# Kernel tuning notes

Hardware: AMD Instinct MI355X
Metric: run time of the kernel (lower is better)

Reference implementation:

```python
import jax, jax.numpy as jnp
import numpy as np

B, F_, J, D = 64, 256, 25, 3
FILT = 64
N = B * F_ * J
EPS = 1e-5


def setup_inputs() -> dict:
    key = jax.random.key(0)
    ks = jax.random.split(key, 20)
    x = jax.random.normal(ks[0], (B, F_, J, D), jnp.float32)
    # block-diagonal skeleton: chain bones, bidirectional, tiled over B*F graphs
    bones = np.stack([np.arange(J - 1), np.arange(1, J)], axis=1)  # (24,2)
    e = np.concatenate([bones, bones[:, ::-1]], axis=0)            # (48,2)
    G = B * F_
    off = (np.arange(G, dtype=np.int64) * J)[:, None, None]
    edge_index = jnp.asarray((e[None].astype(np.int64) + off).reshape(-1, 2).T)  # (2, G*48)
    s = 0.1
    W1 = jax.random.normal(ks[1], (D, FILT), jnp.float32) * s
    b1 = jnp.zeros((FILT,), jnp.float32)
    g1 = jnp.ones((FILT,), jnp.float32)
    be1 = jnp.zeros((FILT,), jnp.float32)
    W2 = jax.random.normal(ks[2], (FILT, FILT), jnp.float32) * s
    b2 = jnp.zeros((FILT,), jnp.float32)
    g2 = jnp.ones((FILT,), jnp.float32)
    be2 = jnp.zeros((FILT,), jnp.float32)
    cw1 = jax.random.normal(ks[3], (2 * FILT, J * FILT, 3), jnp.float32) * 0.02  # OIH
    cb1 = jnp.zeros((2 * FILT,), jnp.float32)
    cg1 = jnp.ones((2 * FILT,), jnp.float32)
    cbe1 = jnp.zeros((2 * FILT,), jnp.float32)
    cw2 = jax.random.normal(ks[4], (FILT, 2 * FILT, 1), jnp.float32) * 0.05
    cb2 = jnp.zeros((FILT,), jnp.float32)
    cg2 = jnp.ones((FILT,), jnp.float32)
    cbe2 = jnp.zeros((FILT,), jnp.float32)
    return dict(x=x, edge_index=edge_index, batch_size=B, frame_l=F_,
                W1=W1, b1=b1, g1=g1, be1=be1, W2=W2, b2=b2, g2=g2, be2=be2,
                cw1=cw1, cb1=cb1, cg1=cg1, cbe1=cbe1,
                cw2=cw2, cb2=cb2, cg2=cg2, cbe2=cbe2)


def _lrelu(v):
    return jnp.where(v >= 0, v, 0.2 * v)


def _bn_nodes(v, g, b):  # BatchNorm1d on (N, C), batch stats
    m = v.mean(0)
    var = v.var(0)
    return g * (v - m) * jax.lax.rsqrt(var + EPS) + b


def _bn_ncl(v, g, b):  # BatchNorm1d on (B, C, L), batch stats
    m = v.mean((0, 2), keepdims=True)
    var = v.var((0, 2), keepdims=True)
    return g[None, :, None] * (v - m) * jax.lax.rsqrt(var + EPS) + b[None, :, None]


def _gcn(h_in, W, b, src, dst, n):
    # PyG GCNConv: h' = D^{-1/2} (A+I) D^{-1/2} h W + b
    h = h_in @ W
    loop = jnp.arange(n, dtype=src.dtype)
    sa = jnp.concatenate([src, loop])
    da = jnp.concatenate([dst, loop])
    deg = jax.ops.segment_sum(jnp.ones(sa.shape[0], h.dtype), da, num_segments=n)
    dinv = jnp.where(deg > 0, jax.lax.rsqrt(deg), 0.0)
    norm = dinv[sa] * dinv[da]
    return jax.ops.segment_sum(h[sa] * norm[:, None], da, num_segments=n) + b


def _conv1d(v, w, pad):  # v:(B,C,L), w:(O,I,K)
    return jax.lax.conv_general_dilated(v, w, window_strides=(1,), padding=((pad, pad),),
                                         dimension_numbers=("NCH", "OIH", "NCH"))


def reference(x, edge_index, batch_size, frame_l, W1, b1, g1, be1, W2, b2, g2, be2,
              cw1, cb1, cg1, cbe1, cw2, cb2, cg2, cbe2):
    src, dst = edge_index[0], edge_index[1]
    n = x.shape[0] * x.shape[1] * x.shape[2]
    h = x.reshape(-1, x.shape[-1])                               # (N, D)
    h = _lrelu(_bn_nodes(_gcn(h, W1, b1, src, dst, n), g1, be1))  # (N, FILT)
    h = _lrelu(_bn_nodes(_gcn(h, W2, b2, src, dst, n), g2, be2))  # (N, FILT)
    t = h.reshape(batch_size, frame_l, -1).transpose(0, 2, 1)     # (B, J*FILT, L)
    t = _lrelu(_bn_ncl(_conv1d(t, cw1, 1) + cb1[None, :, None], cg1, cbe1))  # dropout: eval = identity
    t = _lrelu(_bn_ncl(_conv1d(t, cw2, 0) + cb2[None, :, None], cg2, cbe2))
    return t.transpose(0, 2, 1)                                   # (B, L, FILT)
```

## Files before the change

### kernel.cpp

```cpp
#include <hip/hip_runtime.h>
#include <stdint.h>

#define B_ 64
#define F2_ 256
#define J_ 25
#define FILT_ 64
#define C1_ 1600
#define O1_ 128
#define NN_ 409600
#define MM_ 16384
#define EPSV 1e-5f

typedef short short8 __attribute__((ext_vector_type(8)));
typedef float f32x4 __attribute__((ext_vector_type(4)));

static const size_t WS_Y2T  = 0;
static const size_t WS_XA   = 52838400;
static const size_t WS_WT1  = 57753600;
static const size_t WS_WT2  = 58982400;
static const size_t WS_WT2G = 58998784;
static const size_t WS_Y3   = 59006976;
static const size_t WS_Y4   = 67395584;
static const size_t WS_ST   = 71589888;
#define ST_S9    0
#define ST_SUM2  16
#define ST_SQ2   80
#define ST_SUM3  144
#define ST_SQ3   272
#define ST_SUM4  400
#define ST_SQ4   464
#define ST_S1    528
#define ST_T1    592
#define ST_SC2   656
#define ST_SH2   720
#define ST_SC3   784
#define ST_SH3   912
#define ST_SC4   1040
#define ST_SH4   1104
#define ST_COUNT 1168

__device__ __forceinline__ float bf2f(unsigned int u){
  return __uint_as_float(u << 16);
}
__device__ __forceinline__ unsigned short f2bf(float f){
  unsigned int u = __float_as_uint(f);
  u += 0x7fffu + ((u >> 16) & 1u);
  return (unsigned short)(u >> 16);
}
__device__ __forceinline__ float lrelu(float x){ return fmaxf(x, 0.2f * x); }
__device__ __forceinline__ float wsum(float v){
  #pragma unroll
  for (int off = 32; off > 0; off >>= 1) v += __shfl_down(v, off, 64);
  return v;
}

typedef __attribute__((address_space(3))) unsigned int lds_uint_t;
typedef __attribute__((address_space(1))) const unsigned int glob_uint_t;
__device__ __forceinline__ void gl16(const void* g, void* l){
  __builtin_amdgcn_global_load_lds((glob_uint_t*)g, (lds_uint_t*)l, 16, 0, 0);
}

__global__ __launch_bounds__(256) void k_zpad(unsigned short* __restrict__ y2t){
  int b = blockIdx.x, tid = threadIdx.x;
  if (tid < 200){
    uint4 z = make_uint4(0,0,0,0);
    ((uint4*)(y2t + (size_t)b * 412800))[tid] = z;
    ((uint4*)(y2t + (size_t)b * 412800 + 257 * 1600))[tid] = z;
  }
}

__global__ __launch_bounds__(256) void k_wt(const float* __restrict__ cw1,
                                            const float* __restrict__ W2,
                                            const float* __restrict__ cw2,
                                            unsigned short* __restrict__ wt1,
                                            unsigned short* __restrict__ wt2,
                                            unsigned short* __restrict__ wt2g){
  int blk = blockIdx.x;
  if (blk < 384){
    int k = blk >> 7, o = blk & 127;
    for (int c = threadIdx.x; c < 1600; c += 256)
      wt1[(size_t)(k * 128 + o) * 1600 + c] = f2bf(cw1[(size_t)(o * 1600 + c) * 3 + k]);
  } else if (blk < 416){
    int idx = ((blk - 384) << 8) + threadIdx.x;
    wt2[idx] = f2bf(cw2[idx]);
  } else {
    int idx = ((blk - 416) << 8) + threadIdx.x;
    int f = idx >> 6, cc = idx & 63;
    wt2g[idx] = f2bf(W2[cc * 64 + f]);
  }
}

__global__ __launch_bounds__(256) void k_gcn1(const float* __restrict__ x,
                                              float* __restrict__ xa,
                                              float* __restrict__ S9){
  int n = blockIdx.x * 256 + threadIdx.x;
  int j = n % J_;
  float dj  = (j == 0 || j == J_-1) ? 2.f : 3.f;
  float rdj = rsqrtf(dj);
  const float* xp = x + (size_t)n * 3;
  float wg = 1.f / dj;
  float a0 = xp[0]*wg, a1 = xp[1]*wg, a2 = xp[2]*wg;
  if (j > 0){
    float dm = (j == 1) ? 2.f : 3.f;  float w = rdj * rsqrtf(dm);
    a0 += xp[-3]*w; a1 += xp[-2]*w; a2 += xp[-1]*w;
  }
  if (j < J_-1){
    float dp = (j == J_-2) ? 2.f : 3.f;  float w = rdj * rsqrtf(dp);
    a0 += xp[3]*w; a1 += xp[4]*w; a2 += xp[5]*w;
  }
  float* xo = xa + (size_t)n * 3;
  xo[0] = a0; xo[1] = a1; xo[2] = a2;
  float p[9] = {a0, a1, a2, a0*a0, a0*a1, a0*a2, a1*a1, a1*a2, a2*a2};
  __shared__ float tmp[9][4];
  int wv = threadIdx.x >> 6, ln = threadIdx.x & 63;
  #pragma unroll
  for (int k = 0; k < 9; k++){ float s = wsum(p[k]); if (ln == 0) tmp[k][wv] = s; }
  __syncthreads();
  if (threadIdx.x < 9){
    int k = threadIdx.x;
    atomicAdd(S9 + k, tmp[k][0] + tmp[k][1] + tmp[k][2] + tmp[k][3]);
  }
}

__global__ void k_bn1(const float* __restrict__ S9, const float* __restrict__ W1,
                      const float* __restrict__ b1, const float* __restrict__ g1,
                      const float* __restrict__ be1,
                      float* __restrict__ s1, float* __restrict__ t1){
  int c = threadIdx.x;
  float inv = 1.f / (float)NN_;
  float m0 = S9[0]*inv, m1 = S9[1]*inv, m2 = S9[2]*inv;
  float C00 = S9[3]*inv - m0*m0, C01 = S9[4]*inv - m0*m1, C02 = S9[5]*inv - m0*m2;
  float C11 = S9[6]*inv - m1*m1, C12 = S9[7]*inv - m1*m2, C22 = S9[8]*inv - m2*m2;
  float w0 = W1[c], w1 = W1[64+c], w2 = W1[128+c];
  float mean = m0*w0 + m1*w1 + m2*w2 + b1[c];
  float var  = w0*w0*C00 + w1*w1*C11 + w2*w2*C22
             + 2.f*(w0*w1*C01 + w0*w2*C02 + w1*w2*C12);
  float s = g1[c] * rsqrtf(var + EPSV);
  s1[c] = s;
  t1[c] = be1[c] - s*mean + s*b1[c];
}

#define H1SLICE(ph, js) do { \
  int js_ = (js); \
  _Pragma("unroll") \
  for (int i_ = 0; i_ < 16; i_++){ \
    const float* xp_ = xas + ((size_t)(wl0 + i_) * 25 + js_) * 3; \
    h[ph][i_] = lrelu(fmaf(sS, fmaf(xp_[0], w0c, fmaf(xp_[1], w1c, xp_[2]*w2c)), tT)); \
  } } while(0)

#define AGGW(pm, pc, pp) do { \
  _Pragma("unroll") \
  for (int i_ = 0; i_ < 16; i_++){ \
    float a_ = wgm*h[pm][i_] + wgs*h[pc][i_] + wgp*h[pp][i_]; \
    int row_ = wl0 + i_; \
    *(unsigned short*)(As + row_*128 + ((((lane>>3)) ^ (row_&7))<<4) + ((lane&7)<<1)) = f2bf(a_); \
  } } while(0)

__global__ __launch_bounds__(256) void k_gcn2m(const float* __restrict__ xa,
                                               const float* __restrict__ W1,
                                               const float* __restrict__ s1,
                                               const float* __restrict__ t1,
                                               const float* __restrict__ b2,
                                               const unsigned short* __restrict__ wt2g,
                                               unsigned short* __restrict__ y2t,
                                               float* __restrict__ sum2,
                                               float* __restrict__ sq2){
  __shared__ float xas[4800];
  __shared__ float prm[384];
  __shared__ char As[8192];
  __shared__ char Bs[8192];
  int blk = blockIdx.x;
  int jh = blk & 1;
  int lq = (blk >> 1) & 3;
  int b  = blk >> 3;
  int l0 = lq << 6;
  int tid = threadIdx.x;
  int w = tid >> 6, lane = tid & 63;

  const float* xsrc = xa + (size_t)(b * 256 + l0) * 75;
  #pragma unroll
  for (int i = 0; i < 5; i++){
    int idx = tid + (i << 8);
    if (idx < 1200) ((float4*)xas)[idx] = ((const float4*)xsrc)[idx];
  }
  prm[tid] = (tid < 192) ? W1[tid] : s1[tid - 192];
  if (tid < 128) prm[256 + tid] = (tid < 64) ? t1[tid] : b2[tid - 64];
  #pragma unroll
  for (int i = 0; i < 2; i++){
    int r = (w << 4) + (i << 3) + (lane >> 3);
    int cblk = lane & 7;
    gl16(wt2g + (size_t)r * 64 + (((cblk ^ (r & 7))) << 3),
         Bs + (w << 11) + (i << 10));
  }
  __syncthreads();

  float w0c = prm[lane], w1c = prm[64 + lane], w2c = prm[128 + lane];
  float sS = prm[192 + lane], tT = prm[256 + lane];
  int wm = w >> 1, wn = w & 1;
  int m0 = (wm << 5) + (lane & 15);
  int n0 = (wn << 5) + (lane & 15);
  int kg = lane >> 4;
  float bias0 = prm[320 + n0], bias1 = prm[320 + n0 + 16];
  int wl0 = w << 4;

  float h[3][16];
  int J0 = jh ? 12 : 0;
  int NJ = jh ? 13 : 12;
  #pragma unroll
  for (int i = 0; i < 16; i++) h[2][i] = 0.f;
  H1SLICE(0, J0);
  if (J0 > 0) H1SLICE(2, J0 - 1);

  float ss0 = 0.f, ss1 = 0.f, qq0 = 0.f, qq1 = 0.f;

  #pragma unroll
  for (int jj = 0; jj < 13; jj++){
    if (jj >= NJ) break;
    int j = J0 + jj;
    if (j + 1 <= 24){
      switch ((jj + 1) % 3){
        case 0: H1SLICE(0, j + 1); break;
        case 1: H1SLICE(1, j + 1); break;
        case 2: H1SLICE(2, j + 1); break;
      }
    }
    float dj  = (j == 0 || j == 24) ? 2.f : 3.f;
    float rdj = rsqrtf(dj);
    float wgs = 1.f / dj;
    float wgm = (j > 0)  ? rdj * rsqrtf((j == 1)  ? 2.f : 3.f) : 0.f;
    float wgp = (j < 24) ? rdj * rsqrtf((j == 23) ? 2.f : 3.f) : 0.f;
    switch (jj % 3){
      case 0: AGGW(2, 0, 1); break;
      case 1: AGGW(0, 1, 2); break;
      case 2: AGGW(1, 2, 0); break;
    }
    __syncthreads();
    f32x4 acc[2][2] = {};
    #pragma unroll
    for (int ks = 0; ks < 2; ks++){
      int kb = kg + (ks << 2);
      short8 a0 = *(const short8*)(As + (m0 << 7)        + ((kb ^ (m0 & 7)) << 4));
      short8 a1 = *(const short8*)(As + ((m0 + 16) << 7) + ((kb ^ (m0 & 7)) << 4));
      short8 b0 = *(const short8*)(Bs + (n0 << 7)        + ((kb ^ (n0 & 7)) << 4));
      short8 b1 = *(const short8*)(Bs + ((n0 + 16) << 7) + ((kb ^ (n0 & 7)) << 4));
      acc[0][0] = __builtin_amdgcn_mfma_f32_16x16x32_bf16(a0, b0, acc[0][0], 0, 0, 0);
      acc[0][1] = __builtin_amdgcn_mfma_f32_16x16x32_bf16(a0, b1, acc[0][1], 0, 0, 0);
      acc[1][0] = __builtin_amdgcn_mfma_f32_16x16x32_bf16(a1, b0, acc[1][0], 0, 0, 0);
      acc[1][1] = __builtin_amdgcn_mfma_f32_16x16x32_bf16(a1, b1, acc[1][1], 0, 0, 0);
    }
    __syncthreads();
    int rowb = (wm << 5) + ((lane >> 4) << 2);
    #pragma unroll
    for (int mi = 0; mi < 2; mi++){
      #pragma unroll
      for (int ni = 0; ni < 2; ni++){
        float bias = ni ? bias1 : bias0;
        int f = n0 + (ni << 4);
        #pragma unroll
        for (int r = 0; r < 4; r++){
          float v = acc[mi][ni][r] + bias;
          if (ni){ ss1 += v; qq1 += v * v; } else { ss0 += v; qq0 += v * v; }
          int rl = rowb + (mi << 4) + r;
          y2t[(size_t)(b * 258 + l0 + rl + 1) * 1600 + j * 64 + f] = f2bf(v);
        }
      }
    }
  }
  ss0 += __shfl_xor(ss0, 16, 64); ss0 += __shfl_xor(ss0, 32, 64);
  ss1 += __shfl_xor(ss1, 16, 64); ss1 += __shfl_xor(ss1, 32, 64);
  qq0 += __shfl_xor(qq0, 16, 64); qq0 += __shfl_xor(qq0, 32, 64);
  qq1 += __shfl_xor(qq1, 16, 64); qq1 += __shfl_xor(qq1, 32, 64);
  if ((lane >> 4) == 0){
    atomicAdd(sum2 + n0, ss0);      atomicAdd(sq2 + n0, qq0);
    atomicAdd(sum2 + n0 + 16, ss1); atomicAdd(sq2 + n0 + 16, qq1);
  }
}

__global__ void k_bnp(const float* __restrict__ sum, const float* __restrict__ sq,
                      const float* __restrict__ g, const float* __restrict__ be,
                      float* __restrict__ sc, float* __restrict__ sh, float inv){
  int c = threadIdx.x;
  float mean = sum[c] * inv;
  float var  = sq[c] * inv - mean * mean;
  float s = g[c] * rsqrtf(var + EPSV);
  sc[c] = s; sh[c] = be[c] - s * mean;
}

__global__ __launch_bounds__(256) void k_bnapp2(unsigned short* __restrict__ y2t,
                                                const float* __restrict__ sc2,
                                                const float* __restrict__ sh2){
  for (unsigned idx = blockIdx.x * 256 + threadIdx.x; idx < 3276800u; idx += 524288u){
    unsigned b = idx / 51200u;
    unsigned rem = idx - b * 51200u;
    unsigned l = rem / 200u;
    unsigned cg = rem - l * 200u;
    uint4* p = (uint4*)y2t + ((size_t)b * 258 + l + 1) * 200 + cg;
    unsigned f0 = (cg << 3) & 63u;
    float4 sa = *(const float4*)(sc2 + f0);
    float4 sb = *(const float4*)(sc2 + f0 + 4);
    float4 ha = *(const float4*)(sh2 + f0);
    float4 hb = *(const float4*)(sh2 + f0 + 4);
    float scs[8] = {sa.x,sa.y,sa.z,sa.w,sb.x,sb.y,sb.z,sb.w};
    float shs[8] = {ha.x,ha.y,ha.z,ha.w,hb.x,hb.y,hb.z,hb.w};
    uint4 v = *p;
    unsigned vv[4] = {v.x,v.y,v.z,v.w};
    unsigned r[4];
    #pragma unroll
    for (int i = 0; i < 4; i++){
      float lo = bf2f(vv[i] & 0xffffu);
      float hi = bf2f(vv[i] >> 16);
      lo = lrelu(fmaf(scs[2*i],   lo, shs[2*i]));
      hi = lrelu(fmaf(scs[2*i+1], hi, shs[2*i+1]));
      r[i] = (unsigned)f2bf(lo) | (((unsigned)f2bf(hi)) << 16);
    }
    *p = make_uint4(r[0],r[1],r[2],r[3]);
  }
}

#define NT_ 75
__global__ __launch_bounds__(256) void k_conv1(const unsigned short* __restrict__ y2t,
                                               const unsigned short* __restrict__ wt1,
                                               const float* __restrict__ cb1,
                                               float* __restrict__ y3,
                                               float* __restrict__ sum3,
                                               float* __restrict__ sq3){
  __shared__ char smem[32768];
  int bid = blockIdx.x;
  int blk = ((bid & 7) << 6) | (bid >> 3);
  int b  = blk >> 3;
  int lq = (blk >> 1) & 3;
  int og = blk & 1;
  int l0 = lq << 6;
  int tid = threadIdx.x;
  int w = tid >> 6, lane = tid & 63;
  int wm = w >> 1, wn = w & 1;
  const unsigned short* y2b = y2t + (size_t)b * 412800;
  const unsigned short* wtb = wt1 + (size_t)og * 64 * 1600;

  int rs = (w << 4) + (lane >> 3);
  int cblk = lane & 7;
  int m0 = (wm << 5) + (lane & 15);
  int n0 = (wn << 5) + (lane & 15);
  int kg = lane >> 4;

  f32x4 acc[2][2] = {};

  auto stage = [&](int t, int buf){
    int cc6 = (t * 0x5556) >> 16;
    int k   = t - cc6 * 3;
    int cc  = cc6 << 6;
    const unsigned short* wk = wtb + (size_t)k * 204800;
    #pragma unroll
    for (int i = 0; i < 2; i++){
      int r = rs + (i << 3);
      int sw = (cblk ^ (r & 7)) << 3;
      gl16(y2b + (size_t)(l0 + r + k) * 1600 + cc + sw,
           smem + buf * 16384 + (w << 11) + (i << 10));
      gl16(wk + (size_t)r * 1600 + cc + sw,
           smem + buf * 16384 + 8192 + (w << 11) + (i << 10));
    }
  };

  stage(0, 0);
  __syncthreads();
  #pragma unroll 2
  for (int t = 0; t < NT_; ++t){
    int buf = t & 1;
    if (t + 1 < NT_) stage(t + 1, buf ^ 1);
    const char* Ab = smem + buf * 16384;
    const char* Bb = Ab + 8192;
    #pragma unroll
    for (int ks = 0; ks < 2; ks++){
      int kb = kg + (ks << 2);
      short8 a0 = *(const short8*)(Ab + (m0 << 7)        + ((kb ^ (m0 & 7)) << 4));
      short8 a1 = *(const short8*)(Ab + ((m0 + 16) << 7) + ((kb ^ (m0 & 7)) << 4));
      short8 b0 = *(const short8*)(Bb + (n0 << 7)        + ((kb ^ (n0 & 7)) << 4));
      short8 b1 = *(const short8*)(Bb + ((n0 + 16) << 7) + ((kb ^ (n0 & 7)) << 4));
      acc[0][0] = __builtin_amdgcn_mfma_f32_16x16x32_bf16(a0, b0, acc[0][0], 0, 0, 0);
      acc[0][1] = __builtin_amdgcn_mfma_f32_16x16x32_bf16(a0, b1, acc[0][1], 0, 0, 0);
      acc[1][0] = __builtin_amdgcn_mfma_f32_16x16x32_bf16(a1, b0, acc[1][0], 0, 0, 0);
      acc[1][1] = __builtin_amdgcn_mfma_f32_16x16x32_bf16(a1, b1, acc[1][1], 0, 0, 0);
    }
    __syncthreads();
  }

  int colb = (og << 6) + n0;
  int rowb = l0 + (wm << 5) + ((lane >> 4) << 2);
  float ss0 = 0.f, ss1 = 0.f, qq0 = 0.f, qq1 = 0.f;
  #pragma unroll
  for (int mi = 0; mi < 2; mi++){
    #pragma unroll
    for (int ni = 0; ni < 2; ni++){
      int col = colb + (ni << 4);
      float bias = cb1[col];
      #pragma unroll
      for (int r = 0; r < 4; r++){
        float v = acc[mi][ni][r] + bias;
        if (ni){ ss1 += v; qq1 += v * v; } else { ss0 += v; qq0 += v * v; }
        y3[(size_t)((b << 8) + rowb + (mi << 4) + r) * 128 + col] = v;
      }
    }
  }
  ss0 += __shfl_xor(ss0, 16, 64); ss0 += __shfl_xor(ss0, 32, 64);
  ss1 += __shfl_xor(ss1, 16, 64); ss1 += __shfl_xor(ss1, 32, 64);
  qq0 += __shfl_xor(qq0, 16, 64); qq0 += __shfl_xor(qq0, 32, 64);
  qq1 += __shfl_xor(qq1, 16, 64); qq1 += __shfl_xor(qq1, 32, 64);
  if ((lane >> 4) == 0){
    atomicAdd(sum3 + colb, ss0);      atomicAdd(sq3 + colb, qq0);
    atomicAdd(sum3 + colb + 16, ss1); atomicAdd(sq3 + colb + 16, qq1);
  }
}

__global__ __launch_bounds__(256) void k_conv2(const float* __restrict__ y3,
                                               const float* __restrict__ sc3,
                                               const float* __restrict__ sh3,
                                               const unsigned short* __restrict__ wt2,
                                               const float* __restrict__ cb2,
                                               float* __restrict__ y4,
                                               float* __restrict__ sum4,
                                               float* __restrict__ sq4){
  __shared__ char smem[32768];
  int blk = blockIdx.x;
  int b = blk >> 2, lq = blk & 3;
  int l0 = lq << 6;
  int tid = threadIdx.x;
  int w = tid >> 6, lane = tid & 63;
  int wm = w >> 1, wn = w & 1;
  #pragma unroll
  for (int i = 0; i < 4; i++){
    int r = (w << 4) + (i << 2) + (lane >> 4);
    int sw = (((lane & 15) ^ (r & 7)) << 3);
    gl16(wt2 + (size_t)r * 128 + sw, smem + 16384 + (w << 12) + (i << 10));
  }
  #pragma unroll
  for (int i = 0; i < 4; i++){
    int idx = tid + (i << 8);
    int r = idx >> 4, s = idx & 15;
    const float* src = y3 + (size_t)((b << 8) + l0 + r) * 128 + (s << 3);
    float4 v0 = *(const float4*)(src);
    float4 v1 = *(const float4*)(src + 4);
    float4 c0 = *(const float4*)(sc3 + (s << 3));
    float4 c1 = *(const float4*)(sc3 + (s << 3) + 4);
    float4 h0 = *(const float4*)(sh3 + (s << 3));
    float4 h1 = *(const float4*)(sh3 + (s << 3) + 4);
    uint4 u;
    u.x = (unsigned)f2bf(lrelu(fmaf(c0.x, v0.x, h0.x))) |
          ((unsigned)f2bf(lrelu(fmaf(c0.y, v0.y, h0.y))) << 16);
    u.y = (unsigned)f2bf(lrelu(fmaf(c0.z, v0.z, h0.z))) |
          ((unsigned)f2bf(lrelu(fmaf(c0.w, v0.w, h0.w))) << 16);
    u.z = (unsigned)f2bf(lrelu(fmaf(c1.x, v1.x, h1.x))) |
          ((unsigned)f2bf(lrelu(fmaf(c1.y, v1.y, h1.y))) << 16);
    u.w = (unsigned)f2bf(lrelu(fmaf(c1.z, v1.z, h1.z))) |
          ((unsigned)f2bf(lrelu(fmaf(c1.w, v1.w, h1.w))) << 16);
    *(uint4*)(smem + r * 256 + ((s ^ (r & 7)) << 4)) = u;
  }
  __syncthreads();
  f32x4 acc[2][2] = {};
  int m0 = (wm << 5) + (lane & 15);
  int n0 = (wn << 5) + (lane & 15);
  int kg = lane >> 4;
  const char* Ab = smem;
  const char* Bb = smem + 16384;
  #pragma unroll
  for (int ks = 0; ks < 4; ks++){
    int kb = kg + (ks << 2);
    short8 a0 = *(const short8*)(Ab + (m0 << 8)        + ((kb ^ (m0 & 7)) << 4));
    short8 a1 = *(const short8*)(Ab + ((m0 + 16) << 8) + ((kb ^ (m0 & 7)) << 4));
    short8 b0 = *(const short8*)(Bb + (n0 << 8)        + ((kb ^ (n0 & 7)) << 4));
    short8 b1 = *(const short8*)(Bb + ((n0 + 16) << 8) + ((kb ^ (n0 & 7)) << 4));
    acc[0][0] = __builtin_amdgcn_mfma_f32_16x16x32_bf16(a0, b0, acc[0][0], 0, 0, 0);
    acc[0][1] = __builtin_amdgcn_mfma_f32_16x16x32_bf16(a0, b1, acc[0][1], 0, 0, 0);
    acc[1][0] = __builtin_amdgcn_mfma_f32_16x16x32_bf16(a1, b0, acc[1][0], 0, 0, 0);
    acc[1][1] = __builtin_amdgcn_mfma_f32_16x16x32_bf16(a1, b1, acc[1][1], 0, 0, 0);
  }
  int rowb = l0 + (wm << 5) + ((lane >> 4) << 2);
  float ss0 = 0.f, ss1 = 0.f, qq0 = 0.f, qq1 = 0.f;
  #pragma unroll
  for (int mi = 0; mi < 2; mi++){
    #pragma unroll
    for (int ni = 0; ni < 2; ni++){
      int f = n0 + (ni << 4);
      float bias = cb2[f];
      #pragma unroll
      for (int r = 0; r < 4; r++){
        float v = acc[mi][ni][r] + bias;
        if (ni){ ss1 += v; qq1 += v * v; } else { ss0 += v; qq0 += v * v; }
        y4[(size_t)((b << 8) + rowb + (mi << 4) + r) * 64 + f] = v;
      }
    }
  }
  ss0 += __shfl_xor(ss0, 16, 64); ss0 += __shfl_xor(ss0, 32, 64);
  ss1 += __shfl_xor(ss1, 16, 64); ss1 += __shfl_xor(ss1, 32, 64);
  qq0 += __shfl_xor(qq0, 16, 64); qq0 += __shfl_xor(qq0, 32, 64);
  qq1 += __shfl_xor(qq1, 16, 64); qq1 += __shfl_xor(qq1, 32, 64);
  if ((lane >> 4) == 0){
    atomicAdd(sum4 + n0, ss0);      atomicAdd(sq4 + n0, qq0);
    atomicAdd(sum4 + n0 + 16, ss1); atomicAdd(sq4 + n0 + 16, qq1);
  }
}

__global__ __launch_bounds__(256) void k_final(const float* __restrict__ y4,
                                               const float* __restrict__ sc4,
                                               const float* __restrict__ sh4,
                                               float* __restrict__ out){
  unsigned q = blockIdx.x * 256 + threadIdx.x;
  unsigned f0 = (q & 15) << 2;
  float4 v = ((const float4*)y4)[q];
  float4 sc = *(const float4*)(sc4 + f0);
  float4 sh = *(const float4*)(sh4 + f0);
  v.x = lrelu(fmaf(sc.x, v.x, sh.x));
  v.y = lrelu(fmaf(sc.y, v.y, sh.y));
  v.z = lrelu(fmaf(sc.z, v.z, sh.z));
  v.w = lrelu(fmaf(sc.w, v.w, sh.w));
  ((float4*)out)[q] = v;
}

extern "C" void kernel_launch(void* const* d_in, const int* in_sizes, int n_in,
                              void* d_out, int out_size, void* d_ws, size_t ws_size,
                              hipStream_t stream){
  const float* x    = (const float*)d_in[0];
  const float* W1   = (const float*)d_in[4];
  const float* b1   = (const float*)d_in[5];
  const float* g1   = (const float*)d_in[6];
  const float* be1  = (const float*)d_in[7];
  const float* W2   = (const float*)d_in[8];
  const float* b2   = (const float*)d_in[9];
  const float* g2   = (const float*)d_in[10];
  const float* be2  = (const float*)d_in[11];
  const float* cw1  = (const float*)d_in[12];
  const float* cb1  = (const float*)d_in[13];
  const float* cg1  = (const float*)d_in[14];
  const float* cbe1 = (const float*)d_in[15];
  const float* cw2  = (const float*)d_in[16];
  const float* cb2  = (const float*)d_in[17];
  const float* cg2  = (const float*)d_in[18];
  const float* cbe2 = (const float*)d_in[19];

  char* ws = (char*)d_ws;
  unsigned short* y2t  = (unsigned short*)(ws + WS_Y2T);
  float* xa            = (float*)(ws + WS_XA);
  unsigned short* wt1  = (unsigned short*)(ws + WS_WT1);
  unsigned short* wt2  = (unsigned short*)(ws + WS_WT2);
  unsigned short* wt2g = (unsigned short*)(ws + WS_WT2G);
  float* y3            = (float*)(ws + WS_Y3);
  float* y4            = (float*)(ws + WS_Y4);
  float* st            = (float*)(ws + WS_ST);

  if (ws_size < WS_ST + ST_COUNT * 4) return;

  hipMemsetAsync(st, 0, ST_COUNT * 4, stream);
  k_zpad  <<<64, 256, 0, stream>>>(y2t);
  k_wt    <<<432, 256, 0, stream>>>(cw1, W2, cw2, wt1, wt2, wt2g);
  k_gcn1  <<<1600, 256, 0, stream>>>(x, xa, st + ST_S9);
  k_bn1   <<<1, 64, 0, stream>>>(st + ST_S9, W1, b1, g1, be1, st + ST_S1, st + ST_T1);
  k_gcn2m <<<512, 256, 0, stream>>>(xa, W1, st + ST_S1, st + ST_T1, b2, wt2g,
                                    y2t, st + ST_SUM2, st + ST_SQ2);
  k_bnp   <<<1, 64, 0, stream>>>(st + ST_SUM2, st + ST_SQ2, g2, be2,
                                 st + ST_SC2, st + ST_SH2, 1.f / (float)NN_);
  k_bnapp2<<<2048, 256, 0, stream>>>(y2t, st + ST_SC2, st + ST_SH2);
  k_conv1 <<<512, 256, 0, stream>>>(y2t, wt1, cb1, y3, st + ST_SUM3, st + ST_SQ3);
  k_bnp   <<<1, 128, 0, stream>>>(st + ST_SUM3, st + ST_SQ3, cg1, cbe1,
                                  st + ST_SC3, st + ST_SH3, 1.f / (float)MM_);
  k_conv2 <<<256, 256, 0, stream>>>(y3, st + ST_SC3, st + ST_SH3, wt2, cb2,
                                    y4, st + ST_SUM4, st + ST_SQ4);
  k_bnp   <<<1, 64, 0, stream>>>(st + ST_SUM4, st + ST_SQ4, cg2, cbe2,
                                 st + ST_SC4, st + ST_SH4, 1.f / (float)MM_);
  k_final <<<1024, 256, 0, stream>>>(y4, st + ST_SC4, st + ST_SH4, (float*)d_out);
}
```

Baseline: 177.9 us.

## Fuse BN2 apply into conv1 A-loads and coalesce gcn2m output stores

The separate batch-norm-apply pass over y2t is removed. conv1 now loads A tiles into registers, applies the BN scale/shift and leaky ReLU, zeroes the padding rows, and writes the result to LDS. The global-to-LDS direct loads for A are replaced with this register staging. Separately, the gcn2m epilogue stages results in a swizzled LDS tile so it can write y2t with 16-byte stores instead of scattered 2-byte ones. This saves a full read-modify-write of y2t and one kernel launch, but conv1 now redoes the BN math for every reuse of each row (3 taps times 2 output groups) and loses its async A loads.

```diff
diff --git a/kernel.cpp b/kernel.cpp
--- a/kernel.cpp
+++ b/kernel.cpp
@@ -169,6 +169,7 @@
   __shared__ float prm[384];
   __shared__ char As[8192];
   __shared__ char Bs[8192];
+  __shared__ char Cs[8192];
   int blk = blockIdx.x;
   int jh = blk & 1;
   int lq = (blk >> 1) & 3;
@@ -248,22 +249,32 @@
       acc[1][0] = __builtin_amdgcn_mfma_f32_16x16x32_bf16(a1, b0, acc[1][0], 0, 0, 0);
       acc[1][1] = __builtin_amdgcn_mfma_f32_16x16x32_bf16(a1, b1, acc[1][1], 0, 0, 0);
     }
-    __syncthreads();
-    int rowb = (wm << 5) + ((lane >> 4) << 2);
+    int rowb2 = (wm << 5) + ((lane >> 4) << 2);
     #pragma unroll
     for (int mi = 0; mi < 2; mi++){
       #pragma unroll
       for (int ni = 0; ni < 2; ni++){
         float bias = ni ? bias1 : bias0;
-        int f = n0 + (ni << 4);
+        int col = n0 + (ni << 4);
+        int colgrp = col >> 4;
         #pragma unroll
         for (int r = 0; r < 4; r++){
           float v = acc[mi][ni][r] + bias;
           if (ni){ ss1 += v; qq1 += v * v; } else { ss0 += v; qq0 += v * v; }
-          int rl = rowb + (mi << 4) + r;
-          y2t[(size_t)(b * 258 + l0 + rl + 1) * 1600 + j * 64 + f] = f2bf(v);
+          int row = rowb2 + (mi << 4) + r;
+          *(unsigned short*)(Cs + row * 128 +
+              (((colgrp ^ ((row >> 2) & 3)) << 5) + ((col & 15) << 1))) = f2bf(v);
         }
       }
+    }
+    __syncthreads();
+    #pragma unroll
+    for (int it = 0; it < 2; it++){
+      int idx = tid + (it << 8);
+      int row = idx >> 3, slot = idx & 7;
+      uint4 u = *(const uint4*)(Cs + row * 128 +
+                ((((slot >> 1) ^ ((row >> 2) & 3)) << 5) + ((slot & 1) << 4)));
+      *(uint4*)(y2t + (size_t)(b * 258 + l0 + row + 1) * 1600 + j * 64 + (slot << 3)) = u;
     }
   }
   ss0 += __shfl_xor(ss0, 16, 64); ss0 += __shfl_xor(ss0, 32, 64);
@@ -286,39 +297,10 @@
   sc[c] = s; sh[c] = be[c] - s * mean;
 }
 
-__global__ __launch_bounds__(256) void k_bnapp2(unsigned short* __restrict__ y2t,
-                                                const float* __restrict__ sc2,
-                                                const float* __restrict__ sh2){
-  for (unsigned idx = blockIdx.x * 256 + threadIdx.x; idx < 3276800u; idx += 524288u){
-    unsigned b = idx / 51200u;
-    unsigned rem = idx - b * 51200u;
-    unsigned l = rem / 200u;
-    unsigned cg = rem - l * 200u;
-    uint4* p = (uint4*)y2t + ((size_t)b * 258 + l + 1) * 200 + cg;
-    unsigned f0 = (cg << 3) & 63u;
-    float4 sa = *(const float4*)(sc2 + f0);
-    float4 sb = *(const float4*)(sc2 + f0 + 4);
-    float4 ha = *(const float4*)(sh2 + f0);
-    float4 hb = *(const float4*)(sh2 + f0 + 4);
-    float scs[8] = {sa.x,sa.y,sa.z,sa.w,sb.x,sb.y,sb.z,sb.w};
-    float shs[8] = {ha.x,ha.y,ha.z,ha.w,hb.x,hb.y,hb.z,hb.w};
-    uint4 v = *p;
-    unsigned vv[4] = {v.x,v.y,v.z,v.w};
-    unsigned r[4];
-    #pragma unroll
-    for (int i = 0; i < 4; i++){
-      float lo = bf2f(vv[i] & 0xffffu);
-      float hi = bf2f(vv[i] >> 16);
-      lo = lrelu(fmaf(scs[2*i],   lo, shs[2*i]));
-      hi = lrelu(fmaf(scs[2*i+1], hi, shs[2*i+1]));
-      r[i] = (unsigned)f2bf(lo) | (((unsigned)f2bf(hi)) << 16);
-    }
-    *p = make_uint4(r[0],r[1],r[2],r[3]);
-  }
-}
-
 #define NT_ 75
 __global__ __launch_bounds__(256) void k_conv1(const unsigned short* __restrict__ y2t,
+                                               const float* __restrict__ sc2,
+                                               const float* __restrict__ sh2,
                                                const unsigned short* __restrict__ wt1,
                                                const float* __restrict__ cb1,
                                                float* __restrict__ y3,
@@ -343,9 +325,27 @@
   int n0 = (wn << 5) + (lane & 15);
   int kg = lane >> 4;
 
+  float4 scA = *(const float4*)(sc2 + (cblk << 3));
+  float4 scB = *(const float4*)(sc2 + (cblk << 3) + 4);
+  float4 shA = *(const float4*)(sh2 + (cblk << 3));
+  float4 shB = *(const float4*)(sh2 + (cblk << 3) + 4);
+  float scv[8] = {scA.x,scA.y,scA.z,scA.w,scB.x,scB.y,scB.z,scB.w};
+  float shv[8] = {shA.x,shA.y,shA.z,shA.w,shB.x,shB.y,shB.z,shB.w};
+
   f32x4 acc[2][2] = {};
-
-  auto stage = [&](int t, int buf){
+  uint4 ra[2];
+
+  auto load_A = [&](int t){
+    int cc6 = (t * 0x5556) >> 16;
+    int k   = t - cc6 * 3;
+    int cc  = cc6 << 6;
+    #pragma unroll
+    for (int i = 0; i < 2; i++){
+      int r = rs + (i << 3);
+      ra[i] = *(const uint4*)(y2b + (size_t)(l0 + r + k) * 1600 + cc + (cblk << 3));
+    }
+  };
+  auto stage_B = [&](int t, int buf){
     int cc6 = (t * 0x5556) >> 16;
     int k   = t - cc6 * 3;
     int cc  = cc6 << 6;
@@ -354,19 +354,39 @@
     for (int i = 0; i < 2; i++){
       int r = rs + (i << 3);
       int sw = (cblk ^ (r & 7)) << 3;
-      gl16(y2b + (size_t)(l0 + r + k) * 1600 + cc + sw,
-           smem + buf * 16384 + (w << 11) + (i << 10));
       gl16(wk + (size_t)r * 1600 + cc + sw,
            smem + buf * 16384 + 8192 + (w << 11) + (i << 10));
     }
   };
-
-  stage(0, 0);
+  auto write_A = [&](int t, int buf){
+    int cc6 = (t * 0x5556) >> 16;
+    int k   = t - cc6 * 3;
+    #pragma unroll
+    for (int i = 0; i < 2; i++){
+      int r = rs + (i << 3);
+      int gr = l0 + r + k;
+      uint4 u = ra[i];
+      unsigned vv[4] = {u.x, u.y, u.z, u.w};
+      unsigned o[4];
+      #pragma unroll
+      for (int q = 0; q < 4; q++){
+        float lo = bf2f(vv[q] & 0xffffu);
+        float hi = bf2f(vv[q] >> 16);
+        lo = lrelu(fmaf(scv[2*q],   lo, shv[2*q]));
+        hi = lrelu(fmaf(scv[2*q+1], hi, shv[2*q+1]));
+        o[q] = (unsigned)f2bf(lo) | (((unsigned)f2bf(hi)) << 16);
+      }
+      uint4 ou = make_uint4(o[0], o[1], o[2], o[3]);
+      if (gr == 0 || gr == 257) ou = make_uint4(0,0,0,0);
+      *(uint4*)(smem + buf * 16384 + r * 128 + ((cblk ^ (r & 7)) << 4)) = ou;
+    }
+  };
+
+  load_A(0); stage_B(0, 0); write_A(0, 0);
   __syncthreads();
-  #pragma unroll 2
   for (int t = 0; t < NT_; ++t){
     int buf = t & 1;
-    if (t + 1 < NT_) stage(t + 1, buf ^ 1);
+    if (t + 1 < NT_){ load_A(t + 1); stage_B(t + 1, buf ^ 1); }
     const char* Ab = smem + buf * 16384;
     const char* Bb = Ab + 8192;
     #pragma unroll
@@ -381,6 +401,7 @@
       acc[1][0] = __builtin_amdgcn_mfma_f32_16x16x32_bf16(a1, b0, acc[1][0], 0, 0, 0);
       acc[1][1] = __builtin_amdgcn_mfma_f32_16x16x32_bf16(a1, b1, acc[1][1], 0, 0, 0);
     }
+    if (t + 1 < NT_) write_A(t + 1, buf ^ 1);
     __syncthreads();
   }
 
@@ -557,8 +578,8 @@
                                     y2t, st + ST_SUM2, st + ST_SQ2);
   k_bnp   <<<1, 64, 0, stream>>>(st + ST_SUM2, st + ST_SQ2, g2, be2,
                                  st + ST_SC2, st + ST_SH2, 1.f / (float)NN_);
-  k_bnapp2<<<2048, 256, 0, stream>>>(y2t, st + ST_SC2, st + ST_SH2);
-  k_conv1 <<<512, 256, 0, stream>>>(y2t, wt1, cb1, y3, st + ST_SUM3, st + ST_SQ3);
+  k_conv1 <<<512, 256, 0, stream>>>(y2t, st + ST_SC2, st + ST_SH2, wt1, cb1,
+                                    y3, st + ST_SUM3, st + ST_SQ3);
   k_bnp   <<<1, 128, 0, stream>>>(st + ST_SUM3, st + ST_SQ3, cg1, cbe1,
                                   st + ST_SC3, st + ST_SH3, 1.f / (float)MM_);
   k_conv2 <<<256, 256, 0, stream>>>(y3, st + ST_SC3, st + ST_SH3, wt2, cb2,
```

Result: slower. 198.9 us (+11.8%).

## Store GCN2 output joint-major and give each wave a private GEMM tile

Applied to the files above, without the earlier changes.

The intermediate activation buffer changes from (b, l, j*64+f) to a joint-major (b, j, l, f) layout. GCN2 then writes contiguous 128-byte rows through a per-wave LDS staging tile using uint4 stores, instead of scattered 2-byte global stores. Each wave now computes its own 16x64 output with B fragments held in registers, which removes the block-wide __syncthreads inside the joint loop. The zero-pad, BN-apply and conv1 load addressing are updated to the new layout, and register pressure rises from the cached B fragments.

```diff
diff --git a/kernel.cpp b/kernel.cpp
--- a/kernel.cpp
+++ b/kernel.cpp
@@ -60,12 +60,14 @@
   __builtin_amdgcn_global_load_lds((glob_uint_t*)g, (lds_uint_t*)l, 16, 0, 0);
 }
 
-__global__ __launch_bounds__(256) void k_zpad(unsigned short* __restrict__ y2t){
+__global__ __launch_bounds__(256) void k_zpad(unsigned short* __restrict__ y2j){
   int b = blockIdx.x, tid = threadIdx.x;
-  if (tid < 200){
-    uint4 z = make_uint4(0,0,0,0);
-    ((uint4*)(y2t + (size_t)b * 412800))[tid] = z;
-    ((uint4*)(y2t + (size_t)b * 412800 + 257 * 1600))[tid] = z;
+  for (int i = tid; i < 400; i += 256){
+    int j = i >> 4;
+    int r = (i >> 3) & 1;
+    int s = i & 7;
+    uint4* p = (uint4*)(y2j + ((size_t)(b * 25 + j) * 258 + (r ? 257 : 0)) * 64) + s;
+    *p = make_uint4(0, 0, 0, 0);
   }
 }
 
@@ -152,8 +154,7 @@
   _Pragma("unroll") \
   for (int i_ = 0; i_ < 16; i_++){ \
     float a_ = wgm*h[pm][i_] + wgs*h[pc][i_] + wgp*h[pp][i_]; \
-    int row_ = wl0 + i_; \
-    *(unsigned short*)(As + row_*128 + ((((lane>>3)) ^ (row_&7))<<4) + ((lane&7)<<1)) = f2bf(a_); \
+    *(unsigned short*)(Ab + i_*128 + ((((lane>>3)) ^ (i_&7))<<4) + ((lane&7)<<1)) = f2bf(a_); \
   } } while(0)
 
 __global__ __launch_bounds__(256) void k_gcn2m(const float* __restrict__ xa,
@@ -162,13 +163,14 @@
                                                const float* __restrict__ t1,
                                                const float* __restrict__ b2,
                                                const unsigned short* __restrict__ wt2g,
-                                               unsigned short* __restrict__ y2t,
+                                               unsigned short* __restrict__ y2j,
                                                float* __restrict__ sum2,
                                                float* __restrict__ sq2){
   __shared__ float xas[4800];
   __shared__ float prm[384];
-  __shared__ char As[8192];
   __shared__ char Bs[8192];
+  __shared__ char Aw[4][2048];
+  __shared__ char Cw[4][2048];
   int blk = blockIdx.x;
   int jh = blk & 1;
   int lq = (blk >> 1) & 3;
@@ -194,14 +196,25 @@
   }
   __syncthreads();
 
+  int kgl = lane >> 4;
+  short8 bf[2][4];
+  #pragma unroll
+  for (int ks = 0; ks < 2; ks++){
+    #pragma unroll
+    for (int nf = 0; nf < 4; nf++){
+      int row = (nf << 4) + (lane & 15);
+      int kb = kgl + (ks << 2);
+      bf[ks][nf] = *(const short8*)(Bs + (row << 7) + ((kb ^ (row & 7)) << 4));
+    }
+  }
   float w0c = prm[lane], w1c = prm[64 + lane], w2c = prm[128 + lane];
   float sS = prm[192 + lane], tT = prm[256 + lane];
-  int wm = w >> 1, wn = w & 1;
-  int m0 = (wm << 5) + (lane & 15);
-  int n0 = (wn << 5) + (lane & 15);
-  int kg = lane >> 4;
-  float bias0 = prm[320 + n0], bias1 = prm[320 + n0 + 16];
+  float bias[4];
+  #pragma unroll
+  for (int nf = 0; nf < 4; nf++) bias[nf] = prm[320 + (nf << 4) + (lane & 15)];
   int wl0 = w << 4;
+  char* Ab = Aw[w];
+  char* Cb = Cw[w];
 
   float h[3][16];
   int J0 = jh ? 12 : 0;
@@ -211,7 +224,7 @@
   H1SLICE(0, J0);
   if (J0 > 0) H1SLICE(2, J0 - 1);
 
-  float ss0 = 0.f, ss1 = 0.f, qq0 = 0.f, qq1 = 0.f;
+  float ss[4] = {0,0,0,0}, qq[4] = {0,0,0,0};
 
   #pragma unroll
   for (int jj = 0; jj < 13; jj++){
@@ -234,45 +247,51 @@
       case 1: AGGW(0, 1, 2); break;
       case 2: AGGW(1, 2, 0); break;
     }
-    __syncthreads();
-    f32x4 acc[2][2] = {};
+    f32x4 acc[4] = {};
     #pragma unroll
     for (int ks = 0; ks < 2; ks++){
-      int kb = kg + (ks << 2);
-      short8 a0 = *(const short8*)(As + (m0 << 7)        + ((kb ^ (m0 & 7)) << 4));
-      short8 a1 = *(const short8*)(As + ((m0 + 16) << 7) + ((kb ^ (m0 & 7)) << 4));
-      short8 b0 = *(const short8*)(Bs + (n0 << 7)        + ((kb ^ (n0 & 7)) << 4));
-      short8 b1 = *(const short8*)(Bs + ((n0 + 16) << 7) + ((kb ^ (n0 & 7)) << 4));
-      acc[0][0] = __builtin_amdgcn_mfma_f32_16x16x32_bf16(a0, b0, acc[0][0], 0, 0, 0);
-      acc[0][1] = __builtin_amdgcn_mfma_f32_16x16x32_bf16(a0, b1, acc[0][1], 0, 0, 0);
-      acc[1][0] = __builtin_amdgcn_mfma_f32_16x16x32_bf16(a1, b0, acc[1][0], 0, 0, 0);
-      acc[1][1] = __builtin_amdgcn_mfma_f32_16x16x32_bf16(a1, b1, acc[1][1], 0, 0, 0);
-    }
-    __syncthreads();
-    int rowb = (wm << 5) + ((lane >> 4) << 2);
-    #pragma unroll
-    for (int mi = 0; mi < 2; mi++){
+      int kb = kgl + (ks << 2);
+      int m0w = lane & 15;
+      short8 a = *(const short8*)(Ab + (m0w << 7) + ((kb ^ (m0w & 7)) << 4));
+      acc[0] = __builtin_amdgcn_mfma_f32_16x16x32_bf16(a, bf[ks][0], acc[0], 0, 0, 0);
+      acc[1] = __builtin_amdgcn_mfma_f32_16x16x32_bf16(a, bf[ks][1], acc[1], 0, 0, 0);
+      acc[2] = __builtin_amdgcn_mfma_f32_16x16x32_bf16(a, bf[ks][2], acc[2], 0, 0, 0);
+      acc[3] = __builtin_amdgcn_mfma_f32_16x16x32_bf16(a, bf[ks][3], acc[3], 0, 0, 0);
+    }
+    int rowb = kgl << 2;
+    int col15 = lane & 15;
+    #pragma unroll
+    for (int nf = 0; nf < 4; nf++){
       #pragma unroll
-      for (int ni = 0; ni < 2; ni++){
-        float bias = ni ? bias1 : bias0;
-        int f = n0 + (ni << 4);
-        #pragma unroll
-        for (int r = 0; r < 4; r++){
-          float v = acc[mi][ni][r] + bias;
-          if (ni){ ss1 += v; qq1 += v * v; } else { ss0 += v; qq0 += v * v; }
-          int rl = rowb + (mi << 4) + r;
-          y2t[(size_t)(b * 258 + l0 + rl + 1) * 1600 + j * 64 + f] = f2bf(v);
-        }
+      for (int r = 0; r < 4; r++){
+        float v = acc[nf][r] + bias[nf];
+        ss[nf] += v; qq[nf] += v * v;
+        int row = rowb + r;
+        *(unsigned short*)(Cb + row * 128 +
+            ((nf ^ ((row >> 2) & 3)) << 5) + (col15 << 1)) = f2bf(v);
       }
     }
-  }
-  ss0 += __shfl_xor(ss0, 16, 64); ss0 += __shfl_xor(ss0, 32, 64);
-  ss1 += __shfl_xor(ss1, 16, 64); ss1 += __shfl_xor(ss1, 32, 64);
-  qq0 += __shfl_xor(qq0, 16, 64); qq0 += __shfl_xor(qq0, 32, 64);
-  qq1 += __shfl_xor(qq1, 16, 64); qq1 += __shfl_xor(qq1, 32, 64);
-  if ((lane >> 4) == 0){
-    atomicAdd(sum2 + n0, ss0);      atomicAdd(sq2 + n0, qq0);
-    atomicAdd(sum2 + n0 + 16, ss1); atomicAdd(sq2 + n0 + 16, qq1);
+    unsigned short* dst = y2j + ((size_t)(b * 25 + j) * 258 + l0 + wl0 + 1) * 64;
+    #pragma unroll
+    for (int it = 0; it < 2; it++){
+      int idx = lane + (it << 6);
+      int row = idx >> 3, slot = idx & 7;
+      uint4 u = *(const uint4*)(Cb + row * 128 +
+                ((((slot >> 1) ^ ((row >> 2) & 3)) << 5) + ((slot & 1) << 4)));
+      *(uint4*)(dst + row * 64 + (slot << 3)) = u;
+    }
+  }
+  #pragma unroll
+  for (int nf = 0; nf < 4; nf++){
+    ss[nf] += __shfl_xor(ss[nf], 16, 64); ss[nf] += __shfl_xor(ss[nf], 32, 64);
+    qq[nf] += __shfl_xor(qq[nf], 16, 64); qq[nf] += __shfl_xor(qq[nf], 32, 64);
+  }
+  if (lane < 16){
+    #pragma unroll
+    for (int nf = 0; nf < 4; nf++){
+      atomicAdd(sum2 + (nf << 4) + lane, ss[nf]);
+      atomicAdd(sq2  + (nf << 4) + lane, qq[nf]);
+    }
   }
 }
 
@@ -286,16 +305,16 @@
   sc[c] = s; sh[c] = be[c] - s * mean;
 }
 
-__global__ __launch_bounds__(256) void k_bnapp2(unsigned short* __restrict__ y2t,
+__global__ __launch_bounds__(256) void k_bnapp2(unsigned short* __restrict__ y2j,
                                                 const float* __restrict__ sc2,
                                                 const float* __restrict__ sh2){
   for (unsigned idx = blockIdx.x * 256 + threadIdx.x; idx < 3276800u; idx += 524288u){
-    unsigned b = idx / 51200u;
-    unsigned rem = idx - b * 51200u;
-    unsigned l = rem / 200u;
-    unsigned cg = rem - l * 200u;
-    uint4* p = (uint4*)y2t + ((size_t)b * 258 + l + 1) * 200 + cg;
-    unsigned f0 = (cg << 3) & 63u;
+    unsigned bj = idx >> 11;
+    unsigned rem = idx & 2047u;
+    unsigned l = rem >> 3;
+    unsigned slot = idx & 7u;
+    uint4* p = (uint4*)y2j + ((size_t)bj * 258 + l + 1) * 8 + slot;
+    unsigned f0 = slot << 3;
     float4 sa = *(const float4*)(sc2 + f0);
     float4 sb = *(const float4*)(sc2 + f0 + 4);
     float4 ha = *(const float4*)(sh2 + f0);
@@ -318,7 +337,7 @@
 }
 
 #define NT_ 75
-__global__ __launch_bounds__(256) void k_conv1(const unsigned short* __restrict__ y2t,
+__global__ __launch_bounds__(256) void k_conv1(const unsigned short* __restrict__ y2j,
                                                const unsigned short* __restrict__ wt1,
                                                const float* __restrict__ cb1,
                                                float* __restrict__ y3,
@@ -334,7 +353,7 @@
   int tid = threadIdx.x;
   int w = tid >> 6, lane = tid & 63;
   int wm = w >> 1, wn = w & 1;
-  const unsigned short* y2b = y2t + (size_t)b * 412800;
+  const unsigned short* y2b = y2j + (size_t)b * 412800;
   const unsigned short* wtb = wt1 + (size_t)og * 64 * 1600;
 
   int rs = (w << 4) + (lane >> 3);
@@ -354,7 +373,7 @@
     for (int i = 0; i < 2; i++){
       int r = rs + (i << 3);
       int sw = (cblk ^ (r & 7)) << 3;
-      gl16(y2b + (size_t)(l0 + r + k) * 1600 + cc + sw,
+      gl16(y2b + ((size_t)cc6 * 258 + l0 + r + k) * 64 + sw,
            smem + buf * 16384 + (w << 11) + (i << 10));
       gl16(wk + (size_t)r * 1600 + cc + sw,
            smem + buf * 16384 + 8192 + (w << 11) + (i << 10));
@@ -537,7 +556,7 @@
   const float* cbe2 = (const float*)d_in[19];
 
   char* ws = (char*)d_ws;
-  unsigned short* y2t  = (unsigned short*)(ws + WS_Y2T);
+  unsigned short* y2j  = (unsigned short*)(ws + WS_Y2T);
   float* xa            = (float*)(ws + WS_XA);
   unsigned short* wt1  = (unsigned short*)(ws + WS_WT1);
   unsigned short* wt2  = (unsigned short*)(ws + WS_WT2);
@@ -549,16 +568,16 @@
   if (ws_size < WS_ST + ST_COUNT * 4) return;
 
   hipMemsetAsync(st, 0, ST_COUNT * 4, stream);
-  k_zpad  <<<64, 256, 0, stream>>>(y2t);
+  k_zpad  <<<64, 256, 0, stream>>>(y2j);
   k_wt    <<<432, 256, 0, stream>>>(cw1, W2, cw2, wt1, wt2, wt2g);
   k_gcn1  <<<1600, 256, 0, stream>>>(x, xa, st + ST_S9);
   k_bn1   <<<1, 64, 0, stream>>>(st + ST_S9, W1, b1, g1, be1, st + ST_S1, st + ST_T1);
   k_gcn2m <<<512, 256, 0, stream>>>(xa, W1, st + ST_S1, st + ST_T1, b2, wt2g,
-                                    y2t, st + ST_SUM2, st + ST_SQ2);
+                                    y2j, st + ST_SUM2, st + ST_SQ2);
   k_bnp   <<<1, 64, 0, stream>>>(st + ST_SUM2, st + ST_SQ2, g2, be2,
                                  st + ST_SC2, st + ST_SH2, 1.f / (float)NN_);
-  k_bnapp2<<<2048, 256, 0, stream>>>(y2t, st + ST_SC2, st + ST_SH2);
-  k_conv1 <<<512, 256, 0, stream>>>(y2t, wt1, cb1, y3, st + ST_SUM3, st + ST_SQ3);
+  k_bnapp2<<<2048, 256, 0, stream>>>(y2j, st + ST_SC2, st + ST_SH2);
+  k_conv1 <<<512, 256, 0, stream>>>(y2j, wt1, cb1, y3, st + ST_SUM3, st + ST_SQ3);
   k_bnp   <<<1, 128, 0, stream>>>(st + ST_SUM3, st + ST_SQ3, cg1, cbe1,
                                   st + ST_SC3, st + ST_SH3, 1.f / (float)MM_);
   k_conv2 <<<256, 256, 0, stream>>>(y3, st + ST_SC3, st + ST_SH3, wt2, cb2,
```

After: 202.5 us. +13.8%, slower.
